# Optimization experiments

Measured on AMD Instinct MI355X. Metric: run time of the kernel, lower is better.

Reference implementation:

```python
import jax, jax.numpy as jnp
import numpy as np

T, H, I, E = 8192, 1024, 2816, 8


def setup_inputs() -> dict:
    key = jax.random.key(0)
    k1, k2, k3, k4, k5 = jax.random.split(key, 5)
    s_in = 1.0 / np.sqrt(H)
    s_mid = 1.0 / np.sqrt(I)
    return {
        "x": jax.random.normal(k1, (T, H), dtype=jnp.float32),
        "expert_indices": jax.random.randint(k2, (T,), 0, E),
        "Wg": jax.random.normal(k3, (E, I, H), dtype=jnp.float32) * s_in,
        "Wu": jax.random.normal(k4, (E, I, H), dtype=jnp.float32) * s_in,
        "Wd": jax.random.normal(k5, (E, H, I), dtype=jnp.float32) * s_mid,
    }


def reference(x, expert_indices, Wg, Wu, Wd):
    # Faithful to TPMoEExperts.forward: per-expert 0/1 mask, dense SwiGLU MLP
    # over the full (masked) token batch, masked accumulate into output.
    output = jnp.zeros_like(x)
    for e in range(E):  # small fixed loop over experts (structurally distinct weights)
        mask = (expert_indices == e).astype(x.dtype)[:, None]  # [T,1]
        xi = x * mask                                           # [T,H]
        gate = jax.nn.silu(xi @ Wg[e].T)                        # [T,I]
        up = xi @ Wu[e].T                                       # [T,I]
        out_e = (gate * up) @ Wd[e].T                           # [T,H]
        output = output + out_e * mask
    return output
```

## Files before the change

kernel.cpp:

```cpp
#include <hip/hip_runtime.h>
#include <hip/hip_bf16.h>

#define T_TOK 8192
#define H_DIM 1024
#define I_DIM 2816
#define E_EXP 8

#define BM 128
#define BN 128
#define BK 64
#define MAXTILES (T_TOK / BM + E_EXP)

typedef __bf16 bf16x8 __attribute__((ext_vector_type(8)));
typedef float f32x4 __attribute__((ext_vector_type(4)));

#define SWZ(r, bc) (((r) * (BK * 2)) + (((bc) ^ (((r) & 7) << 4))))

__device__ __forceinline__ void gload16(const void* g, void* l) {
  __builtin_amdgcn_global_load_lds((const __attribute__((address_space(1))) void*)g,
                                   (__attribute__((address_space(3))) void*)l, 16, 0, 0);
}

__device__ __forceinline__ void cvt_store(unsigned char* sm, int off,
                                          const float4& p0, const float4& p1) {
  bf16x8 v;
  v[0] = (__bf16)p0.x; v[1] = (__bf16)p0.y; v[2] = (__bf16)p0.z; v[3] = (__bf16)p0.w;
  v[4] = (__bf16)p1.x; v[5] = (__bf16)p1.y; v[6] = (__bf16)p1.z; v[7] = (__bf16)p1.w;
  *(bf16x8*)(sm + off) = v;
}

__device__ __forceinline__ bf16x8 cvt8(const float4& p0, const float4& p1) {
  bf16x8 v;
  v[0] = (__bf16)p0.x; v[1] = (__bf16)p0.y; v[2] = (__bf16)p0.z; v[3] = (__bf16)p0.w;
  v[4] = (__bf16)p1.x; v[5] = (__bf16)p1.y; v[6] = (__bf16)p1.z; v[7] = (__bf16)p1.w;
  return v;
}

__global__ void k_count(const int* __restrict__ idx, int* __restrict__ counts) {
  int t = blockIdx.x * blockDim.x + threadIdx.x;
  if (t < T_TOK) atomicAdd(&counts[idx[t]], 1);
}

__global__ void k_tiles(const int* __restrict__ counts, int* __restrict__ offsets,
                        int* __restrict__ tE, int* __restrict__ tB,
                        int* __restrict__ tEnd, int* __restrict__ nT) {
  if (threadIdx.x != 0 || blockIdx.x != 0) return;
  int off = 0, nt = 0;
  for (int e = 0; e < E_EXP; ++e) {
    offsets[e] = off;
    int c = counts[e];
    for (int b = 0; b < c; b += BM) { tE[nt] = e; tB[nt] = off + b; tEnd[nt] = off + c; ++nt; }
    off += c;
  }
  offsets[E_EXP] = off;
  *nT = nt;
}

__global__ void k_scatter(const int* __restrict__ idx, const int* __restrict__ offsets,
                          int* __restrict__ cursor, int* __restrict__ order) {
  int t = blockIdx.x * blockDim.x + threadIdx.x;
  if (t < T_TOK) {
    int e = idx[t];
    int p = offsets[e] + atomicAdd(&cursor[e], 1);
    order[p] = t;
  }
}

__global__ __launch_bounds__(256) void k_cvt(const float* __restrict__ src,
                                             __bf16* __restrict__ dst, int n8) {
  int i = blockIdx.x * blockDim.x + threadIdx.x;
  if (i < n8) {
    const float4 p0 = ((const float4*)src)[i * 2];
    const float4 p1 = ((const float4*)src)[i * 2 + 1];
    ((bf16x8*)dst)[i] = cvt8(p0, p1);
  }
}

__global__ __launch_bounds__(128) void k_xperm(const float* __restrict__ x,
                                               const int* __restrict__ order,
                                               __bf16* __restrict__ xp) {
  const int row = blockIdx.x;
  const int tok = order[row];
  const float* s = x + (size_t)tok * H_DIM + threadIdx.x * 8;
  const float4 p0 = ((const float4*)s)[0];
  const float4 p1 = ((const float4*)s)[1];
  *(bf16x8*)(xp + (size_t)row * H_DIM + threadIdx.x * 8) = cvt8(p0, p1);
}

__global__ __launch_bounds__(256) void k_gateup2(
    const __bf16* __restrict__ xp, const __bf16* __restrict__ wg, const __bf16* __restrict__ wu,
    const int* __restrict__ tE, const int* __restrict__ tB,
    const int* __restrict__ tEnd, const int* __restrict__ nT, __bf16* __restrict__ hp) {
  const int tile = blockIdx.y;
  if (tile >= *nT) return;
  const int e = tE[tile];
  const int rowbase = tB[tile];
  const int rowEnd = tEnd[tile];
  const int nbase = blockIdx.x * BN;

  __shared__ __align__(16) unsigned char smA[BM * BK * 2];
  __shared__ __align__(16) unsigned char smG[BN * BK * 2];
  __shared__ __align__(16) unsigned char smU[BN * BK * 2];

  const int tid = threadIdx.x;
  const int lane = tid & 63;
  const int w = tid >> 6;
  const int wm = w >> 1, wn = w & 1;

  const int lrow = lane >> 3;
  const int lchunk = (lane & 7) ^ lrow;
  const __bf16* aptr[4];
  const __bf16* gptr[4];
  const __bf16* uptr[4];
#pragma unroll
  for (int j = 0; j < 4; ++j) {
    const int rl = (w * 4 + j) * 8 + lrow;
    aptr[j] = xp + (size_t)(rowbase + rl) * H_DIM + lchunk * 8;
    gptr[j] = wg + ((size_t)e * I_DIM + nbase + rl) * H_DIM + lchunk * 8;
    uptr[j] = wu + ((size_t)e * I_DIM + nbase + rl) * H_DIM + lchunk * 8;
  }

  f32x4 accg[4][4], accu[4][4];
#pragma unroll
  for (int m = 0; m < 4; ++m)
#pragma unroll
    for (int n = 0; n < 4; ++n)
#pragma unroll
      for (int j = 0; j < 4; ++j) { accg[m][n][j] = 0.f; accu[m][n][j] = 0.f; }

  const int nK = H_DIM / BK;
  for (int kt = 0; kt < nK; ++kt) {
    const int kof = kt * BK;
#pragma unroll
    for (int j = 0; j < 4; ++j) {
      unsigned char* lbase = (unsigned char*)smA + (w * 4 + j) * 1024;
      gload16(aptr[j] + kof, lbase);
      gload16(gptr[j] + kof, (unsigned char*)smG + (w * 4 + j) * 1024);
      gload16(uptr[j] + kof, (unsigned char*)smU + (w * 4 + j) * 1024);
    }
    __syncthreads();
#pragma unroll
    for (int ks = 0; ks < 2; ++ks) {
      bf16x8 a[4], bg[4], bu[4];
#pragma unroll
      for (int m = 0; m < 4; ++m) {
        const int row = wm * 64 + m * 16 + (lane & 15);
        a[m] = *(const bf16x8*)(smA + SWZ(row, ks * 64 + ((lane >> 4) * 16)));
      }
#pragma unroll
      for (int n = 0; n < 4; ++n) {
        const int row = wn * 64 + n * 16 + (lane & 15);
        const int off = SWZ(row, ks * 64 + ((lane >> 4) * 16));
        bg[n] = *(const bf16x8*)(smG + off);
        bu[n] = *(const bf16x8*)(smU + off);
      }
#pragma unroll
      for (int m = 0; m < 4; ++m)
#pragma unroll
        for (int n = 0; n < 4; ++n) {
          accg[m][n] = __builtin_amdgcn_mfma_f32_16x16x32_bf16(a[m], bg[n], accg[m][n], 0, 0, 0);
          accu[m][n] = __builtin_amdgcn_mfma_f32_16x16x32_bf16(a[m], bu[n], accu[m][n], 0, 0, 0);
        }
    }
    __syncthreads();
  }

#pragma unroll
  for (int m = 0; m < 4; ++m) {
    const int row0 = wm * 64 + m * 16 + (lane >> 4) * 4;
#pragma unroll
    for (int j = 0; j < 4; ++j) {
      const int gr = rowbase + row0 + j;
      if (gr < rowEnd) {
        __bf16* dst = hp + (size_t)gr * I_DIM + nbase;
#pragma unroll
        for (int n = 0; n < 4; ++n) {
          const int col = wn * 64 + n * 16 + (lane & 15);
          const float g = accg[m][n][j];
          const float u = accu[m][n][j];
          dst[col] = (__bf16)(g / (1.f + __expf(-g)) * u);
        }
      }
    }
  }
}

__global__ __launch_bounds__(256) void k_down2(
    const __bf16* __restrict__ hp, const __bf16* __restrict__ wd,
    const int* __restrict__ order, const int* __restrict__ tE, const int* __restrict__ tB,
    const int* __restrict__ tEnd, const int* __restrict__ nT, float* __restrict__ out) {
  const int tile = blockIdx.y;
  if (tile >= *nT) return;
  const int e = tE[tile];
  const int rowbase = tB[tile];
  const int rowEnd = tEnd[tile];
  const int nbase = blockIdx.x * BN;

  __shared__ __align__(16) unsigned char smA[BM * BK * 2];
  __shared__ __align__(16) unsigned char smB[BN * BK * 2];

  const int tid = threadIdx.x;
  const int lane = tid & 63;
  const int w = tid >> 6;
  const int wm = w >> 1, wn = w & 1;

  const int lrow = lane >> 3;
  const int lchunk = (lane & 7) ^ lrow;
  const __bf16* aptr[4];
  const __bf16* bptr[4];
#pragma unroll
  for (int j = 0; j < 4; ++j) {
    const int rl = (w * 4 + j) * 8 + lrow;
    aptr[j] = hp + (size_t)(rowbase + rl) * I_DIM + lchunk * 8;
    bptr[j] = wd + ((size_t)e * H_DIM + nbase + rl) * I_DIM + lchunk * 8;
  }

  f32x4 acc[4][4];
#pragma unroll
  for (int m = 0; m < 4; ++m)
#pragma unroll
    for (int n = 0; n < 4; ++n)
#pragma unroll
      for (int j = 0; j < 4; ++j) acc[m][n][j] = 0.f;

  const int nK = I_DIM / BK;
  for (int kt = 0; kt < nK; ++kt) {
    const int kof = kt * BK;
#pragma unroll
    for (int j = 0; j < 4; ++j) {
      gload16(aptr[j] + kof, (unsigned char*)smA + (w * 4 + j) * 1024);
      gload16(bptr[j] + kof, (unsigned char*)smB + (w * 4 + j) * 1024);
    }
    __syncthreads();
#pragma unroll
    for (int ks = 0; ks < 2; ++ks) {
      bf16x8 a[4], b[4];
#pragma unroll
      for (int m = 0; m < 4; ++m) {
        const int row = wm * 64 + m * 16 + (lane & 15);
        a[m] = *(const bf16x8*)(smA + SWZ(row, ks * 64 + ((lane >> 4) * 16)));
      }
#pragma unroll
      for (int n = 0; n < 4; ++n) {
        const int row = wn * 64 + n * 16 + (lane & 15);
        b[n] = *(const bf16x8*)(smB + SWZ(row, ks * 64 + ((lane >> 4) * 16)));
      }
#pragma unroll
      for (int m = 0; m < 4; ++m)
#pragma unroll
        for (int n = 0; n < 4; ++n)
          acc[m][n] = __builtin_amdgcn_mfma_f32_16x16x32_bf16(a[m], b[n], acc[m][n], 0, 0, 0);
    }
    __syncthreads();
  }

#pragma unroll
  for (int m = 0; m < 4; ++m) {
    const int row0 = wm * 64 + m * 16 + (lane >> 4) * 4;
#pragma unroll
    for (int j = 0; j < 4; ++j) {
      const int gr = rowbase + row0 + j;
      if (gr < rowEnd) {
        const int tok = order[gr];
        float* dst = out + (size_t)tok * H_DIM + nbase;
#pragma unroll
        for (int n = 0; n < 4; ++n) {
          const int col = wn * 64 + n * 16 + (lane & 15);
          dst[col] = acc[m][n][j];
        }
      }
    }
  }
}

__global__ __launch_bounds__(256) void k_gateup_f32(
    const float* __restrict__ x, const float* __restrict__ Wg, const float* __restrict__ Wu,
    const int* __restrict__ order, const int* __restrict__ tE, const int* __restrict__ tB,
    const int* __restrict__ tEnd, const int* __restrict__ nT, __bf16* __restrict__ hp) {
  const int tile = blockIdx.y;
  if (tile >= *nT) return;
  const int e = tE[tile];
  const int rowbase = tB[tile];
  const int rowEnd = tEnd[tile];
  const int nbase = blockIdx.x * BN;

  __shared__ __align__(16) unsigned char smA[BM * BK * 2];
  __shared__ __align__(16) unsigned char smG[BN * BK * 2];
  __shared__ __align__(16) unsigned char smU[BN * BK * 2];

  const int tid = threadIdx.x;
  const int lane = tid & 63;
  const int w = tid >> 6;
  const int wm = w >> 1, wn = w & 1;

  const int r = tid >> 1;
  const int c2 = tid & 1;
  const int gr_s = rowbase + r;
  const bool rvalid = gr_s < rowEnd;
  const float* xrow = rvalid ? (x + (size_t)order[gr_s] * H_DIM) : x;
  const float* grow = Wg + ((size_t)e * I_DIM + nbase + r) * H_DIM;
  const float* urow = Wu + ((size_t)e * I_DIM + nbase + r) * H_DIM;

  f32x4 accg[4][4], accu[4][4];
#pragma unroll
  for (int m = 0; m < 4; ++m)
#pragma unroll
    for (int n = 0; n < 4; ++n)
#pragma unroll
      for (int j = 0; j < 4; ++j) { accg[m][n][j] = 0.f; accu[m][n][j] = 0.f; }

  const int nK = H_DIM / BK;
  for (int kt = 0; kt < nK; ++kt) {
    const int kof = kt * BK + c2 * 32;
#pragma unroll
    for (int i = 0; i < 4; ++i) {
      const int off = SWZ(r, c2 * 64 + i * 16);
      if (rvalid) {
        const float4 p0 = *(const float4*)(xrow + kof + i * 8);
        const float4 p1 = *(const float4*)(xrow + kof + i * 8 + 4);
        cvt_store(smA, off, p0, p1);
      } else {
        bf16x8 z;
#pragma unroll
        for (int q = 0; q < 8; ++q) z[q] = (__bf16)0.f;
        *(bf16x8*)(smA + off) = z;
      }
    }
#pragma unroll
    for (int i = 0; i < 4; ++i) {
      const int off = SWZ(r, c2 * 64 + i * 16);
      const float4 g0 = *(const float4*)(grow + kof + i * 8);
      const float4 g1 = *(const float4*)(grow + kof + i * 8 + 4);
      cvt_store(smG, off, g0, g1);
      const float4 u0 = *(const float4*)(urow + kof + i * 8);
      const float4 u1 = *(const float4*)(urow + kof + i * 8 + 4);
      cvt_store(smU, off, u0, u1);
    }
    __syncthreads();
#pragma unroll
    for (int ks = 0; ks < 2; ++ks) {
      bf16x8 a[4], bg[4], bu[4];
#pragma unroll
      for (int m = 0; m < 4; ++m) {
        const int row = wm * 64 + m * 16 + (lane & 15);
        a[m] = *(const bf16x8*)(smA + SWZ(row, ks * 64 + ((lane >> 4) * 16)));
      }
#pragma unroll
      for (int n = 0; n < 4; ++n) {
        const int row = wn * 64 + n * 16 + (lane & 15);
        const int off = SWZ(row, ks * 64 + ((lane >> 4) * 16));
        bg[n] = *(const bf16x8*)(smG + off);
        bu[n] = *(const bf16x8*)(smU + off);
      }
#pragma unroll
      for (int m = 0; m < 4; ++m)
#pragma unroll
        for (int n = 0; n < 4; ++n) {
          accg[m][n] = __builtin_amdgcn_mfma_f32_16x16x32_bf16(a[m], bg[n], accg[m][n], 0, 0, 0);
          accu[m][n] = __builtin_amdgcn_mfma_f32_16x16x32_bf16(a[m], bu[n], accu[m][n], 0, 0, 0);
        }
    }
    __syncthreads();
  }

#pragma unroll
  for (int m = 0; m < 4; ++m) {
    const int row0 = wm * 64 + m * 16 + (lane >> 4) * 4;
#pragma unroll
    for (int j = 0; j < 4; ++j) {
      const int gr = rowbase + row0 + j;
      if (gr < rowEnd) {
        __bf16* dst = hp + (size_t)gr * I_DIM + nbase;
#pragma unroll
        for (int n = 0; n < 4; ++n) {
          const int col = wn * 64 + n * 16 + (lane & 15);
          const float g = accg[m][n][j];
          const float u = accu[m][n][j];
          dst[col] = (__bf16)(g / (1.f + __expf(-g)) * u);
        }
      }
    }
  }
}

__global__ __launch_bounds__(256) void k_down_f32(
    const __bf16* __restrict__ hp, const float* __restrict__ Wd,
    const int* __restrict__ order, const int* __restrict__ tE, const int* __restrict__ tB,
    const int* __restrict__ tEnd, const int* __restrict__ nT, float* __restrict__ out) {
  const int tile = blockIdx.y;
  if (tile >= *nT) return;
  const int e = tE[tile];
  const int rowbase = tB[tile];
  const int rowEnd = tEnd[tile];
  const int nbase = blockIdx.x * BN;

  __shared__ __align__(16) unsigned char smA[BM * BK * 2];
  __shared__ __align__(16) unsigned char smB[BN * BK * 2];

  const int tid = threadIdx.x;
  const int lane = tid & 63;
  const int w = tid >> 6;
  const int wm = w >> 1, wn = w & 1;

  const int r = tid >> 1;
  const int c2 = tid & 1;
  const __bf16* arow = hp + (size_t)(rowbase + r) * I_DIM;
  const float* brow = Wd + ((size_t)e * H_DIM + nbase + r) * I_DIM;

  f32x4 acc[4][4];
#pragma unroll
  for (int m = 0; m < 4; ++m)
#pragma unroll
    for (int n = 0; n < 4; ++n)
#pragma unroll
      for (int j = 0; j < 4; ++j) acc[m][n][j] = 0.f;

  const int nK = I_DIM / BK;
  for (int kt = 0; kt < nK; ++kt) {
#pragma unroll
    for (int i = 0; i < 4; ++i) {
      const bf16x8 v = *(const bf16x8*)(arow + kt * BK + c2 * 32 + i * 8);
      *(bf16x8*)(smA + SWZ(r, c2 * 64 + i * 16)) = v;
    }
    const int kof = kt * BK + c2 * 32;
#pragma unroll
    for (int i = 0; i < 4; ++i) {
      const float4 p0 = *(const float4*)(brow + kof + i * 8);
      const float4 p1 = *(const float4*)(brow + kof + i * 8 + 4);
      cvt_store(smB, SWZ(r, c2 * 64 + i * 16), p0, p1);
    }
    __syncthreads();
#pragma unroll
    for (int ks = 0; ks < 2; ++ks) {
      bf16x8 a[4], b[4];
#pragma unroll
      for (int m = 0; m < 4; ++m) {
        const int row = wm * 64 + m * 16 + (lane & 15);
        a[m] = *(const bf16x8*)(smA + SWZ(row, ks * 64 + ((lane >> 4) * 16)));
      }
#pragma unroll
      for (int n = 0; n < 4; ++n) {
        const int row = wn * 64 + n * 16 + (lane & 15);
        b[n] = *(const bf16x8*)(smB + SWZ(row, ks * 64 + ((lane >> 4) * 16)));
      }
#pragma unroll
      for (int m = 0; m < 4; ++m)
#pragma unroll
        for (int n = 0; n < 4; ++n)
          acc[m][n] = __builtin_amdgcn_mfma_f32_16x16x32_bf16(a[m], b[n], acc[m][n], 0, 0, 0);
    }
    __syncthreads();
  }

#pragma unroll
  for (int m = 0; m < 4; ++m) {
    const int row0 = wm * 64 + m * 16 + (lane >> 4) * 4;
#pragma unroll
    for (int j = 0; j < 4; ++j) {
      const int gr = rowbase + row0 + j;
      if (gr < rowEnd) {
        const int tok = order[gr];
        float* dst = out + (size_t)tok * H_DIM + nbase;
#pragma unroll
        for (int n = 0; n < 4; ++n) {
          const int col = wn * 64 + n * 16 + (lane & 15);
          dst[col] = acc[m][n][j];
        }
      }
    }
  }
}

extern "C" void kernel_launch(void* const* d_in, const int* in_sizes, int n_in,
                              void* d_out, int out_size, void* d_ws, size_t ws_size,
                              hipStream_t stream) {
  const float* x = (const float*)d_in[0];
  const int* eidx = (const int*)d_in[1];
  const float* Wg = (const float*)d_in[2];
  const float* Wu = (const float*)d_in[3];
  const float* Wd = (const float*)d_in[4];
  float* out = (float*)d_out;

  char* ws = (char*)d_ws;
  size_t off = 0;
  auto alloc = [&](size_t bytes) -> void* {
    void* p = ws + off;
    off = (off + bytes + 255) & ~(size_t)255;
    return p;
  };
  const size_t TPAD = T_TOK + BM;
  __bf16* hp = (__bf16*)alloc(TPAD * I_DIM * sizeof(__bf16));
  int* order = (int*)alloc(T_TOK * sizeof(int));
  int* offsets = (int*)alloc((E_EXP + 1) * sizeof(int));
  int* tE = (int*)alloc(MAXTILES * sizeof(int));
  int* tB = (int*)alloc(MAXTILES * sizeof(int));
  int* tEnd = (int*)alloc(MAXTILES * sizeof(int));
  int* nT = (int*)alloc(sizeof(int));
  int* cc = (int*)alloc(2 * E_EXP * sizeof(int));
  int* counts = cc;
  int* cursor = cc + E_EXP;

  const size_t base_need = off;
  const size_t WSZ = (size_t)E_EXP * I_DIM * H_DIM;
  const size_t need_bf16 = base_need + (TPAD * H_DIM + 3 * WSZ) * sizeof(__bf16) + 1024;
  const bool use_bf16 = ws_size >= need_bf16;

  hipMemsetAsync(cc, 0, 2 * E_EXP * sizeof(int), stream);
  k_count<<<T_TOK / 256, 256, 0, stream>>>(eidx, counts);
  k_tiles<<<1, 1, 0, stream>>>(counts, offsets, tE, tB, tEnd, nT);
  k_scatter<<<T_TOK / 256, 256, 0, stream>>>(eidx, offsets, cursor, order);

  if (use_bf16) {
    __bf16* xp = (__bf16*)alloc(TPAD * H_DIM * sizeof(__bf16));
    __bf16* wg16 = (__bf16*)alloc(WSZ * sizeof(__bf16));
    __bf16* wu16 = (__bf16*)alloc(WSZ * sizeof(__bf16));
    __bf16* wd16 = (__bf16*)alloc(WSZ * sizeof(__bf16));
    const int n8 = (int)(WSZ / 8);
    k_cvt<<<(n8 + 255) / 256, 256, 0, stream>>>(Wg, wg16, n8);
    k_cvt<<<(n8 + 255) / 256, 256, 0, stream>>>(Wu, wu16, n8);
    k_cvt<<<(n8 + 255) / 256, 256, 0, stream>>>(Wd, wd16, n8);
    k_xperm<<<T_TOK, 128, 0, stream>>>(x, order, xp);
    k_gateup2<<<dim3(I_DIM / BN, MAXTILES), 256, 0, stream>>>(xp, wg16, wu16, tE, tB, tEnd, nT, hp);
    k_down2<<<dim3(H_DIM / BN, MAXTILES), 256, 0, stream>>>(hp, wd16, order, tE, tB, tEnd, nT, out);
  } else {
    k_gateup_f32<<<dim3(I_DIM / BN, MAXTILES), 256, 0, stream>>>(x, Wg, Wu, order, tE, tB, tEnd, nT, hp);
    k_down_f32<<<dim3(H_DIM / BN, MAXTILES), 256, 0, stream>>>(hp, Wd, order, tE, tB, tEnd, nT, out);
  }
}
```

Baseline: 441.4 us.

## Add double-buffered 512-thread gate/up and down GEMM kernels with dynamic LDS

Adds new gate-up and down kernels that use 8 waves per block, a 2x4 wave layout, and double-buffered LDS tiles in dynamic shared memory. The next K-tile's global-to-LDS loads are issued before the current tile's MFMAs, which removes one barrier per iteration and overlaps memory latency with compute. The fp32 fallback path is dropped and the bf16 workspace is always assumed. Larger LDS use (up to 96 KB) may lower occupancy, and the kernels rely on the dynamic-LDS attribute being accepted.

```diff
diff --git a/kernel.cpp b/kernel.cpp
--- a/kernel.cpp
+++ b/kernel.cpp
@@ -19,14 +19,6 @@
 __device__ __forceinline__ void gload16(const void* g, void* l) {
   __builtin_amdgcn_global_load_lds((const __attribute__((address_space(1))) void*)g,
                                    (__attribute__((address_space(3))) void*)l, 16, 0, 0);
-}
-
-__device__ __forceinline__ void cvt_store(unsigned char* sm, int off,
-                                          const float4& p0, const float4& p1) {
-  bf16x8 v;
-  v[0] = (__bf16)p0.x; v[1] = (__bf16)p0.y; v[2] = (__bf16)p0.z; v[3] = (__bf16)p0.w;
-  v[4] = (__bf16)p1.x; v[5] = (__bf16)p1.y; v[6] = (__bf16)p1.z; v[7] = (__bf16)p1.w;
-  *(bf16x8*)(sm + off) = v;
 }
 
 __device__ __forceinline__ bf16x8 cvt8(const float4& p0, const float4& p1) {
@@ -87,6 +79,222 @@
   *(bf16x8*)(xp + (size_t)row * H_DIM + threadIdx.x * 8) = cvt8(p0, p1);
 }
 
+__global__ __launch_bounds__(512, 2) void k_gateup3(
+    const __bf16* __restrict__ xp, const __bf16* __restrict__ wg, const __bf16* __restrict__ wu,
+    const int* __restrict__ tE, const int* __restrict__ tB,
+    const int* __restrict__ tEnd, const int* __restrict__ nT, __bf16* __restrict__ hp) {
+  const int tile = blockIdx.y;
+  if (tile >= *nT) return;
+  const int e = tE[tile];
+  const int rowbase = tB[tile];
+  const int rowEnd = tEnd[tile];
+  const int nbase = blockIdx.x * BN;
+
+  extern __shared__ __align__(16) unsigned char smem[];
+  unsigned char* smA = smem;
+  unsigned char* smG = smem + 32768;
+  unsigned char* smU = smem + 65536;
+
+  const int tid = threadIdx.x;
+  const int lane = tid & 63;
+  const int w = tid >> 6;
+  const int wm = w & 1, wn = w >> 1;
+
+  const int lr = lane >> 3;
+  const int lc = (lane & 7) ^ lr;
+  const __bf16* aS[2]; const __bf16* gS[2]; const __bf16* uS[2];
+  int ldst[2];
+#pragma unroll
+  for (int r = 0; r < 2; ++r) {
+    const int rt = r * 64 + w * 8 + lr;
+    aS[r] = xp + (size_t)(rowbase + rt) * H_DIM + lc * 8;
+    gS[r] = wg + ((size_t)e * I_DIM + nbase + rt) * H_DIM + lc * 8;
+    uS[r] = wu + ((size_t)e * I_DIM + nbase + rt) * H_DIM + lc * 8;
+    ldst[r] = (r * 64 + w * 8) * 128;
+  }
+
+  f32x4 accg[4][2], accu[4][2];
+#pragma unroll
+  for (int m = 0; m < 4; ++m)
+#pragma unroll
+    for (int n = 0; n < 2; ++n)
+#pragma unroll
+      for (int j = 0; j < 4; ++j) { accg[m][n][j] = 0.f; accu[m][n][j] = 0.f; }
+
+  const int nK = H_DIM / BK;
+#pragma unroll
+  for (int r = 0; r < 2; ++r) {
+    gload16(aS[r], smA + ldst[r]);
+    gload16(gS[r], smG + ldst[r]);
+    gload16(uS[r], smU + ldst[r]);
+  }
+  __syncthreads();
+
+  int cur = 0;
+  for (int kt = 0; kt < nK; ++kt) {
+    if (kt + 1 < nK) {
+      const int kof = (kt + 1) * BK;
+      const int b = (cur ^ 1) * 16384;
+#pragma unroll
+      for (int r = 0; r < 2; ++r) {
+        gload16(aS[r] + kof, smA + b + ldst[r]);
+        gload16(gS[r] + kof, smG + b + ldst[r]);
+        gload16(uS[r] + kof, smU + b + ldst[r]);
+      }
+    }
+    const unsigned char* A = smA + cur * 16384;
+    const unsigned char* G = smG + cur * 16384;
+    const unsigned char* U = smU + cur * 16384;
+#pragma unroll
+    for (int ks = 0; ks < 2; ++ks) {
+      bf16x8 a[4], bg[2], bu[2];
+#pragma unroll
+      for (int m = 0; m < 4; ++m) {
+        const int row = wm * 64 + m * 16 + (lane & 15);
+        a[m] = *(const bf16x8*)(A + SWZ(row, ks * 64 + ((lane >> 4) * 16)));
+      }
+#pragma unroll
+      for (int n = 0; n < 2; ++n) {
+        const int row = wn * 32 + n * 16 + (lane & 15);
+        const int off = SWZ(row, ks * 64 + ((lane >> 4) * 16));
+        bg[n] = *(const bf16x8*)(G + off);
+        bu[n] = *(const bf16x8*)(U + off);
+      }
+#pragma unroll
+      for (int m = 0; m < 4; ++m)
+#pragma unroll
+        for (int n = 0; n < 2; ++n) {
+          accg[m][n] = __builtin_amdgcn_mfma_f32_16x16x32_bf16(a[m], bg[n], accg[m][n], 0, 0, 0);
+          accu[m][n] = __builtin_amdgcn_mfma_f32_16x16x32_bf16(a[m], bu[n], accu[m][n], 0, 0, 0);
+        }
+    }
+    __syncthreads();
+    cur ^= 1;
+  }
+
+#pragma unroll
+  for (int m = 0; m < 4; ++m) {
+    const int row0 = wm * 64 + m * 16 + (lane >> 4) * 4;
+#pragma unroll
+    for (int j = 0; j < 4; ++j) {
+      const int gr = rowbase + row0 + j;
+      if (gr < rowEnd) {
+        __bf16* dst = hp + (size_t)gr * I_DIM + nbase;
+#pragma unroll
+        for (int n = 0; n < 2; ++n) {
+          const int col = wn * 32 + n * 16 + (lane & 15);
+          const float g = accg[m][n][j];
+          const float u = accu[m][n][j];
+          dst[col] = (__bf16)(g / (1.f + __expf(-g)) * u);
+        }
+      }
+    }
+  }
+}
+
+__global__ __launch_bounds__(512, 2) void k_down3(
+    const __bf16* __restrict__ hp, const __bf16* __restrict__ wd,
+    const int* __restrict__ order, const int* __restrict__ tE, const int* __restrict__ tB,
+    const int* __restrict__ tEnd, const int* __restrict__ nT, float* __restrict__ out) {
+  const int tile = blockIdx.y;
+  if (tile >= *nT) return;
+  const int e = tE[tile];
+  const int rowbase = tB[tile];
+  const int rowEnd = tEnd[tile];
+  const int nbase = blockIdx.x * BN;
+
+  extern __shared__ __align__(16) unsigned char smem2[];
+  unsigned char* smA = smem2;
+  unsigned char* smB = smem2 + 32768;
+
+  const int tid = threadIdx.x;
+  const int lane = tid & 63;
+  const int w = tid >> 6;
+  const int wm = w & 1, wn = w >> 1;
+
+  const int lr = lane >> 3;
+  const int lc = (lane & 7) ^ lr;
+  const __bf16* aS[2]; const __bf16* bS[2];
+  int ldst[2];
+#pragma unroll
+  for (int r = 0; r < 2; ++r) {
+    const int rt = r * 64 + w * 8 + lr;
+    aS[r] = hp + (size_t)(rowbase + rt) * I_DIM + lc * 8;
+    bS[r] = wd + ((size_t)e * H_DIM + nbase + rt) * I_DIM + lc * 8;
+    ldst[r] = (r * 64 + w * 8) * 128;
+  }
+
+  f32x4 acc[4][2];
+#pragma unroll
+  for (int m = 0; m < 4; ++m)
+#pragma unroll
+    for (int n = 0; n < 2; ++n)
+#pragma unroll
+      for (int j = 0; j < 4; ++j) acc[m][n][j] = 0.f;
+
+  const int nK = I_DIM / BK;
+#pragma unroll
+  for (int r = 0; r < 2; ++r) {
+    gload16(aS[r], smA + ldst[r]);
+    gload16(bS[r], smB + ldst[r]);
+  }
+  __syncthreads();
+
+  int cur = 0;
+  for (int kt = 0; kt < nK; ++kt) {
+    if (kt + 1 < nK) {
+      const int kof = (kt + 1) * BK;
+      const int b = (cur ^ 1) * 16384;
+#pragma unroll
+      for (int r = 0; r < 2; ++r) {
+        gload16(aS[r] + kof, smA + b + ldst[r]);
+        gload16(bS[r] + kof, smB + b + ldst[r]);
+      }
+    }
+    const unsigned char* A = smA + cur * 16384;
+    const unsigned char* B = smB + cur * 16384;
+#pragma unroll
+    for (int ks = 0; ks < 2; ++ks) {
+      bf16x8 a[4], b[2];
+#pragma unroll
+      for (int m = 0; m < 4; ++m) {
+        const int row = wm * 64 + m * 16 + (lane & 15);
+        a[m] = *(const bf16x8*)(A + SWZ(row, ks * 64 + ((lane >> 4) * 16)));
+      }
+#pragma unroll
+      for (int n = 0; n < 2; ++n) {
+        const int row = wn * 32 + n * 16 + (lane & 15);
+        b[n] = *(const bf16x8*)(B + SWZ(row, ks * 64 + ((lane >> 4) * 16)));
+      }
+#pragma unroll
+      for (int m = 0; m < 4; ++m)
+#pragma unroll
+        for (int n = 0; n < 2; ++n)
+          acc[m][n] = __builtin_amdgcn_mfma_f32_16x16x32_bf16(a[m], b[n], acc[m][n], 0, 0, 0);
+    }
+    __syncthreads();
+    cur ^= 1;
+  }
+
+#pragma unroll
+  for (int m = 0; m < 4; ++m) {
+    const int row0 = wm * 64 + m * 16 + (lane >> 4) * 4;
+#pragma unroll
+    for (int j = 0; j < 4; ++j) {
+      const int gr = rowbase + row0 + j;
+      if (gr < rowEnd) {
+        const int tok = order[gr];
+        float* dst = out + (size_t)tok * H_DIM + nbase;
+#pragma unroll
+        for (int n = 0; n < 2; ++n) {
+          const int col = wn * 32 + n * 16 + (lane & 15);
+          dst[col] = acc[m][n][j];
+        }
+      }
+    }
+  }
+}
+
 __global__ __launch_bounds__(256) void k_gateup2(
     const __bf16* __restrict__ xp, const __bf16* __restrict__ wg, const __bf16* __restrict__ wu,
     const int* __restrict__ tE, const int* __restrict__ tB,
@@ -133,8 +341,7 @@
     const int kof = kt * BK;
 #pragma unroll
     for (int j = 0; j < 4; ++j) {
-      unsigned char* lbase = (unsigned char*)smA + (w * 4 + j) * 1024;
-      gload16(aptr[j] + kof, lbase);
+      gload16(aptr[j] + kof, (unsigned char*)smA + (w * 4 + j) * 1024);
       gload16(gptr[j] + kof, (unsigned char*)smG + (w * 4 + j) * 1024);
       gload16(uptr[j] + kof, (unsigned char*)smU + (w * 4 + j) * 1024);
     }
@@ -230,204 +437,6 @@
     for (int j = 0; j < 4; ++j) {
       gload16(aptr[j] + kof, (unsigned char*)smA + (w * 4 + j) * 1024);
       gload16(bptr[j] + kof, (unsigned char*)smB + (w * 4 + j) * 1024);
-    }
-    __syncthreads();
-#pragma unroll
-    for (int ks = 0; ks < 2; ++ks) {
-      bf16x8 a[4], b[4];
-#pragma unroll
-      for (int m = 0; m < 4; ++m) {
-        const int row = wm * 64 + m * 16 + (lane & 15);
-        a[m] = *(const bf16x8*)(smA + SWZ(row, ks * 64 + ((lane >> 4) * 16)));
-      }
-#pragma unroll
-      for (int n = 0; n < 4; ++n) {
-        const int row = wn * 64 + n * 16 + (lane & 15);
-        b[n] = *(const bf16x8*)(smB + SWZ(row, ks * 64 + ((lane >> 4) * 16)));
-      }
-#pragma unroll
-      for (int m = 0; m < 4; ++m)
-#pragma unroll
-        for (int n = 0; n < 4; ++n)
-          acc[m][n] = __builtin_amdgcn_mfma_f32_16x16x32_bf16(a[m], b[n], acc[m][n], 0, 0, 0);
-    }
-    __syncthreads();
-  }
-
-#pragma unroll
-  for (int m = 0; m < 4; ++m) {
-    const int row0 = wm * 64 + m * 16 + (lane >> 4) * 4;
-#pragma unroll
-    for (int j = 0; j < 4; ++j) {
-      const int gr = rowbase + row0 + j;
-      if (gr < rowEnd) {
-        const int tok = order[gr];
-        float* dst = out + (size_t)tok * H_DIM + nbase;
-#pragma unroll
-        for (int n = 0; n < 4; ++n) {
-          const int col = wn * 64 + n * 16 + (lane & 15);
-          dst[col] = acc[m][n][j];
-        }
-      }
-    }
-  }
-}
-
-__global__ __launch_bounds__(256) void k_gateup_f32(
-    const float* __restrict__ x, const float* __restrict__ Wg, const float* __restrict__ Wu,
-    const int* __restrict__ order, const int* __restrict__ tE, const int* __restrict__ tB,
-    const int* __restrict__ tEnd, const int* __restrict__ nT, __bf16* __restrict__ hp) {
-  const int tile = blockIdx.y;
-  if (tile >= *nT) return;
-  const int e = tE[tile];
-  const int rowbase = tB[tile];
-  const int rowEnd = tEnd[tile];
-  const int nbase = blockIdx.x * BN;
-
-  __shared__ __align__(16) unsigned char smA[BM * BK * 2];
-  __shared__ __align__(16) unsigned char smG[BN * BK * 2];
-  __shared__ __align__(16) unsigned char smU[BN * BK * 2];
-
-  const int tid = threadIdx.x;
-  const int lane = tid & 63;
-  const int w = tid >> 6;
-  const int wm = w >> 1, wn = w & 1;
-
-  const int r = tid >> 1;
-  const int c2 = tid & 1;
-  const int gr_s = rowbase + r;
-  const bool rvalid = gr_s < rowEnd;
-  const float* xrow = rvalid ? (x + (size_t)order[gr_s] * H_DIM) : x;
-  const float* grow = Wg + ((size_t)e * I_DIM + nbase + r) * H_DIM;
-  const float* urow = Wu + ((size_t)e * I_DIM + nbase + r) * H_DIM;
-
-  f32x4 accg[4][4], accu[4][4];
-#pragma unroll
-  for (int m = 0; m < 4; ++m)
-#pragma unroll
-    for (int n = 0; n < 4; ++n)
-#pragma unroll
-      for (int j = 0; j < 4; ++j) { accg[m][n][j] = 0.f; accu[m][n][j] = 0.f; }
-
-  const int nK = H_DIM / BK;
-  for (int kt = 0; kt < nK; ++kt) {
-    const int kof = kt * BK + c2 * 32;
-#pragma unroll
-    for (int i = 0; i < 4; ++i) {
-      const int off = SWZ(r, c2 * 64 + i * 16);
-      if (rvalid) {
-        const float4 p0 = *(const float4*)(xrow + kof + i * 8);
-        const float4 p1 = *(const float4*)(xrow + kof + i * 8 + 4);
-        cvt_store(smA, off, p0, p1);
-      } else {
-        bf16x8 z;
-#pragma unroll
-        for (int q = 0; q < 8; ++q) z[q] = (__bf16)0.f;
-        *(bf16x8*)(smA + off) = z;
-      }
-    }
-#pragma unroll
-    for (int i = 0; i < 4; ++i) {
-      const int off = SWZ(r, c2 * 64 + i * 16);
-      const float4 g0 = *(const float4*)(grow + kof + i * 8);
-      const float4 g1 = *(const float4*)(grow + kof + i * 8 + 4);
-      cvt_store(smG, off, g0, g1);
-      const float4 u0 = *(const float4*)(urow + kof + i * 8);
-      const float4 u1 = *(const float4*)(urow + kof + i * 8 + 4);
-      cvt_store(smU, off, u0, u1);
-    }
-    __syncthreads();
-#pragma unroll
-    for (int ks = 0; ks < 2; ++ks) {
-      bf16x8 a[4], bg[4], bu[4];
-#pragma unroll
-      for (int m = 0; m < 4; ++m) {
-        const int row = wm * 64 + m * 16 + (lane & 15);
-        a[m] = *(const bf16x8*)(smA + SWZ(row, ks * 64 + ((lane >> 4) * 16)));
-      }
-#pragma unroll
-      for (int n = 0; n < 4; ++n) {
-        const int row = wn * 64 + n * 16 + (lane & 15);
-        const int off = SWZ(row, ks * 64 + ((lane >> 4) * 16));
-        bg[n] = *(const bf16x8*)(smG + off);
-        bu[n] = *(const bf16x8*)(smU + off);
-      }
-#pragma unroll
-      for (int m = 0; m < 4; ++m)
-#pragma unroll
-        for (int n = 0; n < 4; ++n) {
-          accg[m][n] = __builtin_amdgcn_mfma_f32_16x16x32_bf16(a[m], bg[n], accg[m][n], 0, 0, 0);
-          accu[m][n] = __builtin_amdgcn_mfma_f32_16x16x32_bf16(a[m], bu[n], accu[m][n], 0, 0, 0);
-        }
-    }
-    __syncthreads();
-  }
-
-#pragma unroll
-  for (int m = 0; m < 4; ++m) {
-    const int row0 = wm * 64 + m * 16 + (lane >> 4) * 4;
-#pragma unroll
-    for (int j = 0; j < 4; ++j) {
-      const int gr = rowbase + row0 + j;
-      if (gr < rowEnd) {
-        __bf16* dst = hp + (size_t)gr * I_DIM + nbase;
-#pragma unroll
-        for (int n = 0; n < 4; ++n) {
-          const int col = wn * 64 + n * 16 + (lane & 15);
-          const float g = accg[m][n][j];
-          const float u = accu[m][n][j];
-          dst[col] = (__bf16)(g / (1.f + __expf(-g)) * u);
-        }
-      }
-    }
-  }
-}
-
-__global__ __launch_bounds__(256) void k_down_f32(
-    const __bf16* __restrict__ hp, const float* __restrict__ Wd,
-    const int* __restrict__ order, const int* __restrict__ tE, const int* __restrict__ tB,
-    const int* __restrict__ tEnd, const int* __restrict__ nT, float* __restrict__ out) {
-  const int tile = blockIdx.y;
-  if (tile >= *nT) return;
-  const int e = tE[tile];
-  const int rowbase = tB[tile];
-  const int rowEnd = tEnd[tile];
-  const int nbase = blockIdx.x * BN;
-
-  __shared__ __align__(16) unsigned char smA[BM * BK * 2];
-  __shared__ __align__(16) unsigned char smB[BN * BK * 2];
-
-  const int tid = threadIdx.x;
-  const int lane = tid & 63;
-  const int w = tid >> 6;
-  const int wm = w >> 1, wn = w & 1;
-
-  const int r = tid >> 1;
-  const int c2 = tid & 1;
-  const __bf16* arow = hp + (size_t)(rowbase + r) * I_DIM;
-  const float* brow = Wd + ((size_t)e * H_DIM + nbase + r) * I_DIM;
-
-  f32x4 acc[4][4];
-#pragma unroll
-  for (int m = 0; m < 4; ++m)
-#pragma unroll
-    for (int n = 0; n < 4; ++n)
-#pragma unroll
-      for (int j = 0; j < 4; ++j) acc[m][n][j] = 0.f;
-
-  const int nK = I_DIM / BK;
-  for (int kt = 0; kt < nK; ++kt) {
-#pragma unroll
-    for (int i = 0; i < 4; ++i) {
-      const bf16x8 v = *(const bf16x8*)(arow + kt * BK + c2 * 32 + i * 8);
-      *(bf16x8*)(smA + SWZ(r, c2 * 64 + i * 16)) = v;
-    }
-    const int kof = kt * BK + c2 * 32;
-#pragma unroll
-    for (int i = 0; i < 4; ++i) {
-      const float4 p0 = *(const float4*)(brow + kof + i * 8);
-      const float4 p1 = *(const float4*)(brow + kof + i * 8 + 4);
-      cvt_store(smB, SWZ(r, c2 * 64 + i * 16), p0, p1);
     }
     __syncthreads();
 #pragma unroll
@@ -500,30 +509,34 @@
   int* counts = cc;
   int* cursor = cc + E_EXP;
 
-  const size_t base_need = off;
   const size_t WSZ = (size_t)E_EXP * I_DIM * H_DIM;
-  const size_t need_bf16 = base_need + (TPAD * H_DIM + 3 * WSZ) * sizeof(__bf16) + 1024;
-  const bool use_bf16 = ws_size >= need_bf16;
+  __bf16* xp = (__bf16*)alloc(TPAD * H_DIM * sizeof(__bf16));
+  __bf16* wg16 = (__bf16*)alloc(WSZ * sizeof(__bf16));
+  __bf16* wu16 = (__bf16*)alloc(WSZ * sizeof(__bf16));
+  __bf16* wd16 = (__bf16*)alloc(WSZ * sizeof(__bf16));
+
+  bool big_lds = true;
+  big_lds &= hipFuncSetAttribute((const void*)k_gateup3,
+                                 hipFuncAttributeMaxDynamicSharedMemorySize, 98304) == hipSuccess;
+  big_lds &= hipFuncSetAttribute((const void*)k_down3,
+                                 hipFuncAttributeMaxDynamicSharedMemorySize, 65536) == hipSuccess;
 
   hipMemsetAsync(cc, 0, 2 * E_EXP * sizeof(int), stream);
   k_count<<<T_TOK / 256, 256, 0, stream>>>(eidx, counts);
   k_tiles<<<1, 1, 0, stream>>>(counts, offsets, tE, tB, tEnd, nT);
   k_scatter<<<T_TOK / 256, 256, 0, stream>>>(eidx, offsets, cursor, order);
 
-  if (use_bf16) {
-    __bf16* xp = (__bf16*)alloc(TPAD * H_DIM * sizeof(__bf16));
-    __bf16* wg16 = (__bf16*)alloc(WSZ * sizeof(__bf16));
-    __bf16* wu16 = (__bf16*)alloc(WSZ * sizeof(__bf16));
-    __bf16* wd16 = (__bf16*)alloc(WSZ * sizeof(__bf16));
-    const int n8 = (int)(WSZ / 8);
-    k_cvt<<<(n8 + 255) / 256, 256, 0, stream>>>(Wg, wg16, n8);
-    k_cvt<<<(n8 + 255) / 256, 256, 0, stream>>>(Wu, wu16, n8);
-    k_cvt<<<(n8 + 255) / 256, 256, 0, stream>>>(Wd, wd16, n8);
-    k_xperm<<<T_TOK, 128, 0, stream>>>(x, order, xp);
+  const int n8 = (int)(WSZ / 8);
+  k_cvt<<<(n8 + 255) / 256, 256, 0, stream>>>(Wg, wg16, n8);
+  k_cvt<<<(n8 + 255) / 256, 256, 0, stream>>>(Wu, wu16, n8);
+  k_cvt<<<(n8 + 255) / 256, 256, 0, stream>>>(Wd, wd16, n8);
+  k_xperm<<<T_TOK, 128, 0, stream>>>(x, order, xp);
+
+  if (big_lds) {
+    k_gateup3<<<dim3(I_DIM / BN, MAXTILES), 512, 98304, stream>>>(xp, wg16, wu16, tE, tB, tEnd, nT, hp);
+    k_down3<<<dim3(H_DIM / BN, MAXTILES), 512, 65536, stream>>>(hp, wd16, order, tE, tB, tEnd, nT, out);
+  } else {
     k_gateup2<<<dim3(I_DIM / BN, MAXTILES), 256, 0, stream>>>(xp, wg16, wu16, tE, tB, tEnd, nT, hp);
     k_down2<<<dim3(H_DIM / BN, MAXTILES), 256, 0, stream>>>(hp, wd16, order, tE, tB, tEnd, nT, out);
-  } else {
-    k_gateup_f32<<<dim3(I_DIM / BN, MAXTILES), 256, 0, stream>>>(x, Wg, Wu, order, tE, tB, tEnd, nT, hp);
-    k_down_f32<<<dim3(H_DIM / BN, MAXTILES), 256, 0, stream>>>(hp, Wd, order, tE, tB, tEnd, nT, out);
-  }
-}
+  }
+}
```

After: 386.6 us. 12.4% less time.
